# Performance work log

Measured on AMD Instinct MI355X. Metric: run time of the kernel, lower is better.

The kernel has to match this reference:

```python
import jax, jax.numpy as jnp
import numpy as np

B, C = 4096, 10000


def setup_inputs() -> dict:
    key = jax.random.key(0)
    k1, k2, k3, k4, k5 = jax.random.split(key, 5)
    return {
        "outputs1": jax.random.normal(k1, (B, C), jnp.float32),
        "outputs2": jax.random.normal(k2, (B, C), jnp.float32),
        "outputs3": jax.random.normal(k3, (B, C), jnp.float32),
        "out_s": jax.random.normal(k4, (B, C), jnp.float32),
        "targets": jax.random.randint(k5, (B,), 0, C),
    }


def _margin(out, targets):
    # top1 - top2 if the target class is the argmax, else 0  -> [B]
    top2 = jax.lax.top_k(out, 2)[0]                              # [B, 2]
    tgt = jnp.take_along_axis(out, targets[:, None], axis=1)[:, 0]
    return jnp.where(tgt == top2[:, 0], top2[:, 0] - top2[:, 1], jnp.zeros_like(tgt))


def reference(outputs1, outputs2, outputs3, out_s, targets):
    T_THR = 2.0   # Threshold_weights3 temperature
    T_KD = 20.0   # KL_divergence temperature
    ALPHA = 0.8

    mimic = (outputs1 + outputs2 + outputs3) / 3.0
    teachers = (outputs1, outputs2, outputs3, mimic)

    # per-sample confidence margins for each teacher -> softmax ensemble weights [B,4]
    d = jnp.stack([_margin(t, targets) for t in teachers], axis=1)
    out_threshold = jax.nn.softmax(d / T_THR, axis=1)

    # global max over the three real teachers (scalar)
    max_preds = jnp.maximum(jnp.max(outputs1), jnp.maximum(jnp.max(outputs2), jnp.max(outputs3)))

    # per-sample student CE (shared across teachers)
    ce = -jnp.take_along_axis(jax.nn.log_softmax(out_s, axis=1), targets[:, None], axis=1)[:, 0]
    logp_s = jax.nn.log_softmax(out_s / T_KD, axis=1)

    def loss_for(teacher):
        w = jnp.take_along_axis(teacher, targets[:, None], axis=1)[:, 0] / max_preds
        kd = -jnp.sum(jax.nn.softmax(teacher / T_KD, axis=1) * logp_s, axis=1) * (T_KD * T_KD)
        return (1.0 - ALPHA * w) * ce + (ALPHA * w) * kd

    losses = jnp.stack([loss_for(t) for t in teachers], axis=1)  # [B,4]
    return jnp.mean(jnp.sum(out_threshold * losses, axis=1))
```

## Files before the change

### kernel.cpp

```cpp
#include <hip/hip_runtime.h>

namespace {
constexpr int kB = 4096;
constexpr int kC = 10000;
constexpr int kC4 = kC / 4;
constexpr int kNT = 256;
}

__device__ __forceinline__ float wave_sum(float v) {
#pragma unroll
  for (int o = 32; o > 0; o >>= 1) v += __shfl_down(v, o, 64);
  return v;
}

__device__ __forceinline__ double wave_sum_d(double v) {
#pragma unroll
  for (int o = 32; o > 0; o >>= 1) v += __shfl_down(v, o, 64);
  return v;
}

__device__ __forceinline__ float wave_max(float v) {
#pragma unroll
  for (int o = 32; o > 0; o >>= 1) v = fmaxf(v, __shfl_down(v, o, 64));
  return v;
}

__device__ __forceinline__ void wave_top2(float& m1, float& m2) {
#pragma unroll
  for (int o = 32; o > 0; o >>= 1) {
    float a1 = __shfl_down(m1, o, 64);
    float a2 = __shfl_down(m2, o, 64);
    float lo = fminf(m1, a1);
    m1 = fmaxf(m1, a1);
    m2 = fmaxf(lo, fmaxf(m2, a2));
  }
}

__global__ __launch_bounds__(kNT, 4) void mt3_row_kernel(
    const float* __restrict__ g1, const float* __restrict__ g2,
    const float* __restrict__ g3, const float* __restrict__ gs,
    const int* __restrict__ gt,
    float* __restrict__ ceArr, float* __restrict__ bArr,
    float* __restrict__ mArr) {
  const int b = blockIdx.x;
  const int tid = threadIdx.x;
  const int lane = tid & 63;
  const int wv = tid >> 6;

  const size_t rowOff = (size_t)b * kC;
  const float4* __restrict__ p1 = reinterpret_cast<const float4*>(g1 + rowOff);
  const float4* __restrict__ p2 = reinterpret_cast<const float4*>(g2 + rowOff);
  const float4* __restrict__ p3 = reinterpret_cast<const float4*>(g3 + rowOff);
  const float4* __restrict__ ps = reinterpret_cast<const float4*>(gs + rowOff);

  const int target = gt[b];

  float tv1 = 0.f, tv2 = 0.f, tv3 = 0.f, tvs = 0.f;
  if (tid == 0) {
    tv1 = g1[rowOff + target];
    tv2 = g2[rowOff + target];
    tv3 = g3[rowOff + target];
    tvs = gs[rowOff + target];
  }

  float m1[4], m2[4], Z[4], D[4];
#pragma unroll
  for (int t = 0; t < 4; t++) { m1[t] = -1e30f; m2[t] = -1e30f; Z[t] = 0.f; D[t] = 0.f; }
  float Z1 = 0.f;
  float Z20 = 0.f;

  __shared__ float sZ[4][4], sD[4][4], sM1[4][4], sM2[4][4], sZ1[4], sZ20[4];

  int c = tid;
  float4 A = p1[c], Bv = p2[c], Cv = p3[c], Sv = ps[c];
  while (true) {
    const int cn = c + kNT;
    const bool last = (cn >= kC4);
    const int cl = last ? c : cn;
    float4 nA = p1[cl];
    float4 nB = p2[cl];
    float4 nC = p3[cl];
    float4 nS = ps[cl];

    float va[4] = {A.x, A.y, A.z, A.w};
    float vb[4] = {Bv.x, Bv.y, Bv.z, Bv.w};
    float vc[4] = {Cv.x, Cv.y, Cv.z, Cv.w};
    float vs[4] = {Sv.x, Sv.y, Sv.z, Sv.w};
#pragma unroll
    for (int j = 0; j < 4; j++) {
      const float mim = (va[j] + vb[j] + vc[j]) * (1.0f / 3.0f);
      const float tv[4] = {va[j], vb[j], vc[j], mim};
      const float sv = vs[j];
#pragma unroll
      for (int t = 0; t < 4; t++) {
        const float x = tv[t];
        const float lo = fminf(x, m1[t]);
        m1[t] = fmaxf(x, m1[t]);
        m2[t] = fmaxf(m2[t], lo);
        const float e = __expf(x * 0.05f);
        Z[t] += e;
        D[t] = fmaf(e, sv, D[t]);
      }
      Z1 += __expf(sv);
      Z20 += __expf(sv * 0.05f);
    }

    if (last) break;
    c = cn;
    A = nA; Bv = nB; Cv = nC; Sv = nS;
  }

#pragma unroll
  for (int t = 0; t < 4; t++) {
    Z[t] = wave_sum(Z[t]);
    D[t] = wave_sum(D[t]);
    wave_top2(m1[t], m2[t]);
  }
  Z1 = wave_sum(Z1);
  Z20 = wave_sum(Z20);

  if (lane == 0) {
#pragma unroll
    for (int t = 0; t < 4; t++) {
      sZ[t][wv] = Z[t]; sD[t][wv] = D[t];
      sM1[t][wv] = m1[t]; sM2[t][wv] = m2[t];
    }
    sZ1[wv] = Z1; sZ20[wv] = Z20;
  }
  __syncthreads();

  if (tid == 0) {
    float fZ[4], fD[4], fM1[4], fM2[4];
    float fZ1 = 0.f, fZ20 = 0.f;
#pragma unroll
    for (int t = 0; t < 4; t++) { fZ[t] = 0.f; fD[t] = 0.f; fM1[t] = -1e30f; fM2[t] = -1e30f; }
#pragma unroll
    for (int w = 0; w < 4; w++) {
      fZ1 += sZ1[w]; fZ20 += sZ20[w];
#pragma unroll
      for (int t = 0; t < 4; t++) {
        fZ[t] += sZ[t][w];
        fD[t] += sD[t][w];
        const float a1 = sM1[t][w], a2 = sM2[t][w];
        const float lo = fminf(fM1[t], a1);
        fM1[t] = fmaxf(fM1[t], a1);
        fM2[t] = fmaxf(lo, fmaxf(fM2[t], a2));
      }
    }

    const float tvm = (tv1 + tv2 + tv3) * (1.0f / 3.0f);
    const float tval[4] = {tv1, tv2, tv3, tvm};

    const float ce = logf(fZ1) - tvs;
    const float lz20 = logf(fZ20);

    float d[4], kd[4];
#pragma unroll
    for (int t = 0; t < 4; t++) {
      kd[t] = 400.0f * (lz20 - fD[t] / (20.0f * fZ[t]));
      d[t] = (tval[t] == fM1[t]) ? (fM1[t] - fM2[t]) : 0.0f;
    }
    float ew[4], se = 0.f;
#pragma unroll
    for (int t = 0; t < 4; t++) { ew[t] = __expf(d[t] * 0.5f); se += ew[t]; }
    float rowB = 0.f;
#pragma unroll
    for (int t = 0; t < 4; t++) rowB += (ew[t] / se) * tval[t] * (kd[t] - ce);

    ceArr[b] = ce;
    bArr[b] = rowB;
    mArr[b] = fmaxf(fM1[0], fmaxf(fM1[1], fM1[2]));
  }
}

__global__ __launch_bounds__(256) void mt3_finalize(
    const float* __restrict__ ceArr, const float* __restrict__ bArr,
    const float* __restrict__ mArr, float* __restrict__ out) {
  const int tid = threadIdx.x;
  const int lane = tid & 63;
  const int wv = tid >> 6;

  double sc = 0.0, sb = 0.0;
  float mx = -1e30f;
  for (int i = tid; i < kB; i += 256) {
    sc += (double)ceArr[i];
    sb += (double)bArr[i];
    mx = fmaxf(mx, mArr[i]);
  }
  sc = wave_sum_d(sc);
  sb = wave_sum_d(sb);
  mx = wave_max(mx);

  __shared__ double dsc[4], dsb[4];
  __shared__ float dmx[4];
  if (lane == 0) { dsc[wv] = sc; dsb[wv] = sb; dmx[wv] = mx; }
  __syncthreads();
  if (tid == 0) {
    double A = 0.0, Bc = 0.0;
    float M = -1e30f;
#pragma unroll
    for (int w = 0; w < 4; w++) { A += dsc[w]; Bc += dsb[w]; M = fmaxf(M, dmx[w]); }
    out[0] = (float)((A + 0.8 * Bc / (double)M) / (double)kB);
  }
}

extern "C" void kernel_launch(void* const* d_in, const int* in_sizes, int n_in,
                              void* d_out, int out_size, void* d_ws, size_t ws_size,
                              hipStream_t stream) {
  const float* o1 = (const float*)d_in[0];
  const float* o2 = (const float*)d_in[1];
  const float* o3 = (const float*)d_in[2];
  const float* os = (const float*)d_in[3];
  const int* tg = (const int*)d_in[4];

  float* ws = (float*)d_ws;
  float* ceArr = ws;
  float* bArr = ws + kB;
  float* mArr = ws + 2 * kB;

  mt3_row_kernel<<<kB, kNT, 0, stream>>>(o1, o2, o3, os, tg, ceArr, bArr, mArr);
  mt3_finalize<<<1, 256, 0, stream>>>(ceArr, bArr, mArr, (float*)d_out);
}
```

Before: 517.3 us.

## Stage row loads through LDS with async global-to-LDS double buffering

Replaces the register-level prefetch of the next float4 from each of the four inputs with `__builtin_amdgcn_global_load_lds` copies into a double-buffered LDS staging area, synchronised with a block barrier at each stage. The aim is to free vector registers and let loads for the next tile land in LDS while the current tile is reduced. In exchange, each block now uses 32 KB of LDS and a barrier per stage, which can cap occupancy. Prefetch depth stays at one stage ahead. The reduction scratch space reuses the staging buffer.

```diff
diff --git a/kernel.cpp b/kernel.cpp
--- a/kernel.cpp
+++ b/kernel.cpp
@@ -5,6 +5,7 @@
 constexpr int kC = 10000;
 constexpr int kC4 = kC / 4;
 constexpr int kNT = 256;
+constexpr int kStages = (kC4 + kNT - 1) / kNT;
 }
 
 __device__ __forceinline__ float wave_sum(float v) {
@@ -36,12 +37,20 @@
   }
 }
 
-__global__ __launch_bounds__(kNT, 4) void mt3_row_kernel(
+__device__ __forceinline__ void async_copy16(const float4* g, float4* l) {
+  __builtin_amdgcn_global_load_lds(
+      (const __attribute__((address_space(1))) void*)g,
+      (__attribute__((address_space(3))) void*)l, 16, 0, 0);
+}
+
+__global__ __launch_bounds__(kNT) void mt3_row_kernel(
     const float* __restrict__ g1, const float* __restrict__ g2,
     const float* __restrict__ g3, const float* __restrict__ gs,
     const int* __restrict__ gt,
     float* __restrict__ ceArr, float* __restrict__ bArr,
     float* __restrict__ mArr) {
+  __shared__ float4 stage[2][4][kNT];
+
   const int b = blockIdx.x;
   const int tid = threadIdx.x;
   const int lane = tid & 63;
@@ -69,45 +78,53 @@
   float Z1 = 0.f;
   float Z20 = 0.f;
 
-  __shared__ float sZ[4][4], sD[4][4], sM1[4][4], sM2[4][4], sZ1[4], sZ20[4];
-
-  int c = tid;
-  float4 A = p1[c], Bv = p2[c], Cv = p3[c], Sv = ps[c];
-  while (true) {
-    const int cn = c + kNT;
-    const bool last = (cn >= kC4);
-    const int cl = last ? c : cn;
-    float4 nA = p1[cl];
-    float4 nB = p2[cl];
-    float4 nC = p3[cl];
-    float4 nS = ps[cl];
-
-    float va[4] = {A.x, A.y, A.z, A.w};
-    float vb[4] = {Bv.x, Bv.y, Bv.z, Bv.w};
-    float vc[4] = {Cv.x, Cv.y, Cv.z, Cv.w};
-    float vs[4] = {Sv.x, Sv.y, Sv.z, Sv.w};
-#pragma unroll
-    for (int j = 0; j < 4; j++) {
-      const float mim = (va[j] + vb[j] + vc[j]) * (1.0f / 3.0f);
-      const float tv[4] = {va[j], vb[j], vc[j], mim};
-      const float sv = vs[j];
-#pragma unroll
-      for (int t = 0; t < 4; t++) {
-        const float x = tv[t];
-        const float lo = fminf(x, m1[t]);
-        m1[t] = fmaxf(x, m1[t]);
-        m2[t] = fmaxf(m2[t], lo);
-        const float e = __expf(x * 0.05f);
-        Z[t] += e;
-        D[t] = fmaf(e, sv, D[t]);
+  async_copy16(p1 + tid, &stage[0][0][tid]);
+  async_copy16(p2 + tid, &stage[0][1][tid]);
+  async_copy16(p3 + tid, &stage[0][2][tid]);
+  async_copy16(ps + tid, &stage[0][3][tid]);
+
+  for (int s = 0; s < kStages; ++s) {
+    const int buf = s & 1;
+    __syncthreads();
+
+    if (s + 1 < kStages) {
+      const int gn = (s + 1) * kNT + tid;
+      const int gc = (gn < kC4) ? gn : (kC4 - 1);
+      const int nb = buf ^ 1;
+      async_copy16(p1 + gc, &stage[nb][0][tid]);
+      async_copy16(p2 + gc, &stage[nb][1][tid]);
+      async_copy16(p3 + gc, &stage[nb][2][tid]);
+      async_copy16(ps + gc, &stage[nb][3][tid]);
+    }
+
+    if (s * kNT + tid < kC4) {
+      const float4 A = stage[buf][0][tid];
+      const float4 Bv = stage[buf][1][tid];
+      const float4 Cv = stage[buf][2][tid];
+      const float4 Sv = stage[buf][3][tid];
+      const float va[4] = {A.x, A.y, A.z, A.w};
+      const float vb[4] = {Bv.x, Bv.y, Bv.z, Bv.w};
+      const float vc[4] = {Cv.x, Cv.y, Cv.z, Cv.w};
+      const float vs[4] = {Sv.x, Sv.y, Sv.z, Sv.w};
+#pragma unroll
+      for (int j = 0; j < 4; j++) {
+        const float mim = (va[j] + vb[j] + vc[j]) * (1.0f / 3.0f);
+        const float tv[4] = {va[j], vb[j], vc[j], mim};
+        const float sv = vs[j];
+#pragma unroll
+        for (int t = 0; t < 4; t++) {
+          const float x = tv[t];
+          const float lo = fminf(x, m1[t]);
+          m1[t] = fmaxf(x, m1[t]);
+          m2[t] = fmaxf(m2[t], lo);
+          const float e = __expf(x * 0.05f);
+          Z[t] += e;
+          D[t] = fmaf(e, sv, D[t]);
+        }
+        Z1 += __expf(sv);
+        Z20 += __expf(sv * 0.05f);
       }
-      Z1 += __expf(sv);
-      Z20 += __expf(sv * 0.05f);
-    }
-
-    if (last) break;
-    c = cn;
-    A = nA; Bv = nB; Cv = nC; Sv = nS;
+    }
   }
 
 #pragma unroll
@@ -119,13 +136,18 @@
   Z1 = wave_sum(Z1);
   Z20 = wave_sum(Z20);
 
+  __syncthreads();
+  float* red = reinterpret_cast<float*>(&stage[0][0][0]);
   if (lane == 0) {
 #pragma unroll
     for (int t = 0; t < 4; t++) {
-      sZ[t][wv] = Z[t]; sD[t][wv] = D[t];
-      sM1[t][wv] = m1[t]; sM2[t][wv] = m2[t];
-    }
-    sZ1[wv] = Z1; sZ20[wv] = Z20;
+      red[t * 4 + wv] = Z[t];
+      red[16 + t * 4 + wv] = D[t];
+      red[32 + t * 4 + wv] = m1[t];
+      red[48 + t * 4 + wv] = m2[t];
+    }
+    red[64 + wv] = Z1;
+    red[68 + wv] = Z20;
   }
   __syncthreads();
 
@@ -136,12 +158,13 @@
     for (int t = 0; t < 4; t++) { fZ[t] = 0.f; fD[t] = 0.f; fM1[t] = -1e30f; fM2[t] = -1e30f; }
 #pragma unroll
     for (int w = 0; w < 4; w++) {
-      fZ1 += sZ1[w]; fZ20 += sZ20[w];
+      fZ1 += red[64 + w];
+      fZ20 += red[68 + w];
 #pragma unroll
       for (int t = 0; t < 4; t++) {
-        fZ[t] += sZ[t][w];
-        fD[t] += sD[t][w];
-        const float a1 = sM1[t][w], a2 = sM2[t][w];
+        fZ[t] += red[t * 4 + w];
+        fD[t] += red[16 + t * 4 + w];
+        const float a1 = red[32 + t * 4 + w], a2 = red[48 + t * 4 + w];
         const float lo = fminf(fM1[t], a1);
         fM1[t] = fmaxf(fM1[t], a1);
         fM2[t] = fmaxf(lo, fmaxf(fM2[t], a2));
```

New measurement: 525.5 us. No clear change (+1.6%).
